# Optimization experiments

Measured on AMD Instinct MI355X. Metric: run time of the kernel, lower is better.

Reference implementation:

```python
import jax, jax.numpy as jnp
import numpy as np

N, E, B = 50000, 100000, 512   # nodes, edges, graphs
H, F_NODE, F_EDGE, T_OUT = 64, 16, 8, 1
T = 3                           # message-passing steps


def setup_inputs() -> dict:
    key = jax.random.key(0)
    ks = jax.random.split(key, 18)

    def w(k, shape, fan_in):
        return jax.random.normal(k, shape, dtype=jnp.float32) / np.sqrt(fan_in)

    return {
        "node_features": jax.random.normal(ks[0], (N, F_NODE), dtype=jnp.float32),
        "edge_features": jax.random.normal(ks[1], (E, F_EDGE), dtype=jnp.float32),
        "Esrc": jax.random.randint(ks[2], (E,), 0, N, dtype=jnp.int32),
        "Etgt": jax.random.randint(ks[3], (E,), 0, N, dtype=jnp.int32),
        "batch": jnp.sort(jax.random.randint(ks[4], (N,), 0, B, dtype=jnp.int32)),
        # input linear: node_features -> hidden
        "Win": w(ks[5], (H, F_NODE), F_NODE),
        "bin_": jnp.zeros((H,), jnp.float32),
        # edge encoder MLP: edge_features -> hidden -> hidden*hidden
        "We1": w(ks[6], (H, F_EDGE), F_EDGE),
        "be1": jnp.zeros((H,), jnp.float32),
        "We2": w(ks[7], (H * H, H), H),
        "be2": jnp.zeros((H * H,), jnp.float32),
        # GRU cell (shared across T steps)
        "Wih": w(ks[8], (3 * H, H), H),
        "bih": jnp.zeros((3 * H,), jnp.float32),
        "Whh": w(ks[9], (3 * H, H), H),
        "bhh": jnp.zeros((3 * H,), jnp.float32),
        # output linear: hidden -> target_features
        "Wout": w(ks[10], (T_OUT, H), H),
        "bout": jnp.zeros((T_OUT,), jnp.float32),
    }


def _gru(x, h, Wih, bih, Whh, bhh):
    gi = x @ Wih.T + bih            # [N, 3H]
    gh = h @ Whh.T + bhh
    i_r, i_z, i_n = jnp.split(gi, 3, axis=-1)
    h_r, h_z, h_n = jnp.split(gh, 3, axis=-1)
    r = jax.nn.sigmoid(i_r + h_r)
    z = jax.nn.sigmoid(i_z + h_z)
    n = jnp.tanh(i_n + r * h_n)
    return (1.0 - z) * n + z * h


def reference(node_features, edge_features, Esrc, Etgt, batch,
              Win, bin_, We1, be1, We2, be2,
              Wih, bih, Whh, bhh, Wout, bout):
    # Edge encoder MLP -> per-edge [H, H] message matrix (ENN style)
    eh = jax.nn.relu(edge_features @ We1.T + be1)          # [E, H]
    edge_data = (eh @ We2.T + be2).reshape(E, H, H)        # [E, H, H]

    x = node_features @ Win.T + bin_                       # [N, H]

    for _ in range(T):  # small fixed layer count
        msg = jnp.einsum('eij,ej->ei', edge_data, x[Esrc])  # per-edge matvec
        agg = jax.ops.segment_sum(msg, Etgt, num_segments=N)
        x = _gru(agg, x, Wih, bih, Whh, bhh)

    out = x @ Wout.T + bout                                # [N, 1]
    pooled = jax.ops.segment_sum(out, batch, num_segments=B)  # [B, 1]
    return pooled
```

## Files before the change

### kernel.cpp

```cpp
#include <hip/hip_runtime.h>
#include <hip/hip_fp16.h>

#define NN 50000
#define NE 100000
#define NB 512

typedef _Float16 f16x8 __attribute__((ext_vector_type(8)));
typedef _Float16 f16x4 __attribute__((ext_vector_type(4)));
typedef float f32x4  __attribute__((ext_vector_type(4)));
typedef float f32x16 __attribute__((ext_vector_type(16)));

__device__ __forceinline__ float sigm(float v) { return 1.0f / (1.0f + __expf(-v)); }
__device__ __forceinline__ float tanh_fast(float v) {
    float e = __expf(-2.0f * fabsf(v));
    float t = (1.0f - e) / (1.0f + e);
    return v < 0.f ? -t : t;
}

__global__ void fill0_kernel(float4* __restrict__ p, int n4)
{
    int i = blockIdx.x * 256 + threadIdx.x;
    const int stride = gridDim.x * 256;
    for (; i < n4; i += stride) p[i] = make_float4(0.f, 0.f, 0.f, 0.f);
}

__global__ __launch_bounds__(256) void node_in_kernel(
    const float* __restrict__ nf, const float* __restrict__ Win,
    const float* __restrict__ bin_, float* __restrict__ x, __half* __restrict__ xh)
{
    int idx = blockIdx.x * 256 + threadIdx.x;
    if (idx >= NN * 64) return;
    int n = idx >> 6, h = idx & 63;
    float acc = bin_[h];
    #pragma unroll
    for (int f = 0; f < 16; f++) acc += nf[n * 16 + f] * Win[h * 16 + f];
    x[idx] = acc;
    xh[idx] = __float2half(acc);
}

__global__ __launch_bounds__(256) void edge_l1_kernel(
    const float* __restrict__ ef, const float* __restrict__ We1,
    const float* __restrict__ be1, __half* __restrict__ ehh)
{
    int idx = blockIdx.x * 256 + threadIdx.x;
    if (idx >= NE * 64) return;
    int e = idx >> 6, k = idx & 63;
    float acc = be1[k];
    #pragma unroll
    for (int f = 0; f < 8; f++) acc += ef[e * 8 + f] * We1[k * 8 + f];
    ehh[idx] = __float2half(fmaxf(acc, 0.0f));
}

__global__ __launch_bounds__(256) void pack_b32_kernel(
    const float* __restrict__ We2, const float* __restrict__ be2,
    __half* __restrict__ Bp)
{
    int idx = blockIdx.x * 256 + threadIdx.x;
    if (idx >= 260 * 1024) return;
    int i  = idx & 7;
    int n  = (idx >> 3) & 31;
    int hi = (idx >> 8) & 1;
    int nt = (idx >> 9) & 1;
    int kt = idx >> 10;
    int p  = kt * 16 + hi * 8 + i;
    int col = nt * 32 + n;
    float v;
    if (p < 4096) {
        int j = p >> 6, k = p & 63;
        v = We2[((size_t)(col * 64 + j)) * 64 + k];
    } else {
        v = be2[col * 64 + (p - 4096)];
    }
    Bp[idx] = __float2half(v);
}

__global__ __launch_bounds__(256) void pack_gru_kernel(
    const float* __restrict__ Wih, const float* __restrict__ Whh,
    __half* __restrict__ WG)
{
    int idx = blockIdx.x * 256 + threadIdx.x;
    if (idx >= 24576) return;
    int kk = idx & 31;
    int n  = (idx >> 5) & 15;
    int nt = (idx >> 9) % 24;
    int kt = (idx >> 9) / 24;
    int k = kt * 32 + kk;
    int col192 = (nt % 12) * 16 + n;
    int gate = col192 >> 6, h = col192 & 63;
    const float* src = (nt < 12) ? Wih : Whh;
    WG[idx] = __float2half(src[((size_t)(gate * 64 + h)) * 64 + k]);
}

__global__ __launch_bounds__(256, 2) void msg_kernel(
    const __half* __restrict__ xh, const __half* __restrict__ ehh,
    const __half* __restrict__ Bp,
    const int* __restrict__ Esrc, const int* __restrict__ Etgt,
    float* __restrict__ agg)
{
    __shared__ __attribute__((aligned(16))) __half xs[256 * 72];
    __shared__ __attribute__((aligned(16))) __half bst[16 * 1024];
    __shared__ int tgt_s[256];
    const int tid = threadIdx.x;
    const int e0 = blockIdx.x * 256;
    const int w = tid >> 6, lane = tid & 63;
    const int n32 = lane & 31, hi = lane >> 5;

    {
        const int e = e0 + tid;
        const bool ok = (e < NE);
        const int src = ok ? Esrc[e] : 0;
        tgt_s[tid] = ok ? Etgt[e] : -1;
        const uint4* xsrc = (const uint4*)(xh + (size_t)src * 64);
        #pragma unroll
        for (int i = 0; i < 8; i++) {
            uint4 v = ok ? xsrc[i] : make_uint4(0, 0, 0, 0);
            *(uint4*)(&xs[tid * 72 + i * 8]) = v;
        }
    }

    __half2 ehc[2][4][4];
    #pragma unroll
    for (int mt = 0; mt < 2; mt++) {
        const int e = e0 + w * 64 + mt * 32 + n32;
        if (e < NE) {
            #pragma unroll
            for (int c4 = 0; c4 < 4; c4++) {
                union { uint4 u; __half2 h[4]; } u;
                u.u = *(const uint4*)(ehh + (size_t)e * 64 + c4 * 16 + hi * 8);
                #pragma unroll
                for (int q = 0; q < 4; q++) ehc[mt][c4][q] = u.h[q];
            }
        } else {
            __half2 z = __half2half2(__float2half(0.f));
            #pragma unroll
            for (int c4 = 0; c4 < 4; c4++)
                #pragma unroll
                for (int q = 0; q < 4; q++) ehc[mt][c4][q] = z;
        }
    }

    f32x16 acc[2][2];
    #pragma unroll
    for (int a = 0; a < 2; a++)
        #pragma unroll
        for (int b = 0; b < 2; b++)
            #pragma unroll
            for (int q = 0; q < 16; q++) acc[a][b][q] = 0.f;

    const int rowA0 = w * 64 + n32;
    const __half* blane = bst + hi * 256 + n32 * 8;

    #pragma unroll 1
    for (int c = 0; c < 17; c++) {
        const int nkt = (c < 16) ? 16 : 4;
        __syncthreads();
        {
            const __half* gsrc = Bp + (size_t)c * 16384;
            for (int i = 0; i < nkt / 2; i++)
                *(uint4*)(bst + (size_t)(i * 256 + tid) * 8) =
                    *(const uint4*)(gsrc + (size_t)(i * 256 + tid) * 8);
        }
        __syncthreads();

        if (c < 16) {
            f16x4 xr4[2];
            #pragma unroll
            for (int mt = 0; mt < 2; mt++)
                xr4[mt] = *(const f16x4*)(xs + (rowA0 + mt * 32) * 72 + c * 4);
            #pragma unroll
            for (int u = 0; u < 16; u++) {
                f16x8 b0 = *(const f16x8*)(blane + u * 1024);
                f16x8 b1 = *(const f16x8*)(blane + u * 1024 + 512);
                const int c4 = u & 3;
                const int jq = u >> 2;
                #pragma unroll
                for (int mt = 0; mt < 2; mt++) {
                    union { f16x4 v; __half h[4]; } xu; xu.v = xr4[mt];
                    __half2 xv2 = __half2half2(xu.h[jq]);
                    union { __half2 h[4]; f16x8 v; } a;
                    #pragma unroll
                    for (int q = 0; q < 4; q++) a.h[q] = __hmul2(xv2, ehc[mt][c4][q]);
                    acc[mt][0] = __builtin_amdgcn_mfma_f32_32x32x16_f16(a.v, b0, acc[mt][0], 0, 0, 0);
                    acc[mt][1] = __builtin_amdgcn_mfma_f32_32x32x16_f16(a.v, b1, acc[mt][1], 0, 0, 0);
                }
            }
        } else {
            #pragma unroll
            for (int u = 0; u < 4; u++) {
                f16x8 b0 = *(const f16x8*)(blane + u * 1024);
                f16x8 b1 = *(const f16x8*)(blane + u * 1024 + 512);
                #pragma unroll
                for (int mt = 0; mt < 2; mt++) {
                    f16x8 a = *(const f16x8*)(xs + (rowA0 + mt * 32) * 72 + u * 16 + hi * 8);
                    acc[mt][0] = __builtin_amdgcn_mfma_f32_32x32x16_f16(a, b0, acc[mt][0], 0, 0, 0);
                    acc[mt][1] = __builtin_amdgcn_mfma_f32_32x32x16_f16(a, b1, acc[mt][1], 0, 0, 0);
                }
            }
        }
    }

    #pragma unroll
    for (int mt = 0; mt < 2; mt++) {
        #pragma unroll
        for (int r = 0; r < 16; r++) {
            const int rowe = (r & 3) + 8 * (r >> 2) + 4 * hi;
            const int t = tgt_s[w * 64 + mt * 32 + rowe];
            if (t >= 0) {
                atomicAdd(agg + (size_t)t * 64 + n32, acc[mt][0][r]);
                atomicAdd(agg + (size_t)t * 64 + 32 + n32, acc[mt][1][r]);
            }
        }
    }
}

__global__ __launch_bounds__(256, 3) void gru_kernel(
    const float* __restrict__ agg, float* __restrict__ x, __half* __restrict__ xh,
    const __half* __restrict__ WG,
    const float* __restrict__ bih, const float* __restrict__ bhh)
{
    __shared__ __attribute__((aligned(16))) __half wlds[24576];
    const int tid = threadIdx.x;
    {
        const uint4* src = (const uint4*)WG;
        uint4* dst = (uint4*)wlds;
        #pragma unroll
        for (int i = 0; i < 12; i++) dst[i * 256 + tid] = src[i * 256 + tid];
    }
    __syncthreads();

    const int w = tid >> 6, lane = tid & 63, m = lane & 15, quad = lane >> 4;

    #pragma unroll 1
    for (int tile = blockIdx.x; tile < (NN + 63) / 64; tile += 512) {
        const int nbase = tile * 64 + w * 16;
        const int anode = nbase + m;
        const bool aok = (anode < NN);

        f16x8 a_agg[2], a_x[2];
        #pragma unroll
        for (int kt = 0; kt < 2; kt++) {
            const int koff = kt * 32 + quad * 8;
            if (aok) {
                const float* ap = agg + (size_t)anode * 64 + koff;
                float4 f0 = *(const float4*)ap;
                float4 f1 = *(const float4*)(ap + 4);
                union { __half2 h[4]; f16x8 v; } u;
                u.h[0] = __floats2half2_rn(f0.x, f0.y);
                u.h[1] = __floats2half2_rn(f0.z, f0.w);
                u.h[2] = __floats2half2_rn(f1.x, f1.y);
                u.h[3] = __floats2half2_rn(f1.z, f1.w);
                a_agg[kt] = u.v;
                a_x[kt] = *(const f16x8*)(xh + (size_t)anode * 64 + koff);
            } else {
                f16x8 z;
                #pragma unroll
                for (int i = 0; i < 8; i++) z[i] = (_Float16)0;
                a_agg[kt] = z; a_x[kt] = z;
            }
        }

        f32x4 acc[24];
        #pragma unroll
        for (int nt = 0; nt < 24; nt++)
            #pragma unroll
            for (int q = 0; q < 4; q++) acc[nt][q] = 0.f;

        #pragma unroll
        for (int kt = 0; kt < 2; kt++) {
            #pragma unroll
            for (int nt = 0; nt < 24; nt++) {
                f16x8 b = *(const f16x8*)(wlds + (kt * 24 + nt) * 512 + m * 32 + quad * 8);
                acc[nt] = __builtin_amdgcn_mfma_f32_16x16x32_f16(
                    (nt < 12) ? a_agg[kt] : a_x[kt], b, acc[nt], 0, 0, 0);
            }
        }

        #pragma unroll
        for (int t = 0; t < 4; t++) {
            const int h = t * 16 + m;
            const float bir = bih[h], biz = bih[64 + h], bin = bih[128 + h];
            const float bhr = bhh[h], bhz = bhh[64 + h], bhn = bhh[128 + h];
            #pragma unroll
            for (int r = 0; r < 4; r++) {
                const int nd = nbase + quad * 4 + r;
                if (nd >= NN) continue;
                float ir  = acc[t][r]      + bir;
                float iz  = acc[4 + t][r]  + biz;
                float in_ = acc[8 + t][r]  + bin;
                float hr  = acc[12 + t][r] + bhr;
                float hz  = acc[16 + t][r] + bhz;
                float hn  = acc[20 + t][r] + bhn;
                float rg = sigm(ir + hr);
                float z  = sigm(iz + hz);
                float n  = tanh_fast(in_ + rg * hn);
                float xold = x[(size_t)nd * 64 + h];
                float xn = (1.0f - z) * n + z * xold;
                x[(size_t)nd * 64 + h] = xn;
                xh[(size_t)nd * 64 + h] = __float2half(xn);
            }
        }
    }
}

__global__ __launch_bounds__(256) void pool_kernel(
    const float* __restrict__ x, const float* __restrict__ Wout,
    const float* __restrict__ bout, const int* __restrict__ batch,
    float* __restrict__ out)
{
    const int node = blockIdx.x * 256 + threadIdx.x;
    if (node >= NN) return;
    float acc = bout[0];
    const float4* xp = (const float4*)(x + (size_t)node * 64);
    #pragma unroll
    for (int i = 0; i < 16; i++) {
        float4 v = xp[i];
        acc += v.x * Wout[4*i] + v.y * Wout[4*i+1] + v.z * Wout[4*i+2] + v.w * Wout[4*i+3];
    }
    atomicAdd(out + batch[node], acc);
}

extern "C" void kernel_launch(void* const* d_in, const int* in_sizes, int n_in,
                              void* d_out, int out_size, void* d_ws, size_t ws_size,
                              hipStream_t stream)
{
    const float* nf   = (const float*)d_in[0];
    const float* ef   = (const float*)d_in[1];
    const int*   Esrc = (const int*)  d_in[2];
    const int*   Etgt = (const int*)  d_in[3];
    const int*   bat  = (const int*)  d_in[4];
    const float* Win  = (const float*)d_in[5];
    const float* bin_ = (const float*)d_in[6];
    const float* We1  = (const float*)d_in[7];
    const float* be1  = (const float*)d_in[8];
    const float* We2  = (const float*)d_in[9];
    const float* be2  = (const float*)d_in[10];
    const float* Wih  = (const float*)d_in[11];
    const float* bih  = (const float*)d_in[12];
    const float* Whh  = (const float*)d_in[13];
    const float* bhh  = (const float*)d_in[14];
    const float* Wout = (const float*)d_in[15];
    const float* bout = (const float*)d_in[16];

    char* ws = (char*)d_ws;
    float*  x   = (float*)(ws);
    float*  agg = (float*)(ws + 12800000);
    __half* xh  = (__half*)(ws + 25600000);
    __half* ehh = (__half*)(ws + 32000000);
    __half* Bp  = (__half*)(ws + 44800000);
    __half* WG  = (__half*)(ws + 45400064);

    hipMemsetAsync(d_out, 0, NB * sizeof(float), stream);

    node_in_kernel<<<(NN * 64 + 255) / 256, 256, 0, stream>>>(nf, Win, bin_, x, xh);
    edge_l1_kernel<<<(NE * 64 + 255) / 256, 256, 0, stream>>>(ef, We1, be1, ehh);
    pack_b32_kernel<<<(260 * 1024 + 255) / 256, 256, 0, stream>>>(We2, be2, Bp);
    pack_gru_kernel<<<(24576 + 255) / 256, 256, 0, stream>>>(Wih, Whh, WG);

    for (int t = 0; t < 3; t++) {
        fill0_kernel<<<1024, 256, 0, stream>>>((float4*)agg, NN * 16);
        msg_kernel<<<(NE + 255) / 256, 256, 0, stream>>>(xh, ehh, Bp, Esrc, Etgt, agg);
        gru_kernel<<<512, 256, 0, stream>>>(agg, x, xh, WG, bih, bhh);
    }

    pool_kernel<<<(NN + 255) / 256, 256, 0, stream>>>(x, Wout, bout, bat, (float*)d_out);
}
```

Before: 551.0 us.

## Shrink msg blocks to one wave and stage GRU tiles through LDS

```diff
diff --git a/kernel.cpp b/kernel.cpp
--- a/kernel.cpp
+++ b/kernel.cpp
@@ -91,37 +91,38 @@
     WG[idx] = __float2half(src[((size_t)(gate * 64 + h)) * 64 + k]);
 }
 
-__global__ __launch_bounds__(256, 2) void msg_kernel(
+__global__ __launch_bounds__(64, 1) void msg_kernel(
     const __half* __restrict__ xh, const __half* __restrict__ ehh,
     const __half* __restrict__ Bp,
     const int* __restrict__ Esrc, const int* __restrict__ Etgt,
     float* __restrict__ agg)
 {
-    __shared__ __attribute__((aligned(16))) __half xs[256 * 72];
+    __shared__ __attribute__((aligned(16))) __half xs[128 * 72];
     __shared__ __attribute__((aligned(16))) __half bst[16 * 1024];
-    __shared__ int tgt_s[256];
-    const int tid = threadIdx.x;
-    const int e0 = blockIdx.x * 256;
-    const int w = tid >> 6, lane = tid & 63;
+    __shared__ int tgt_s[128];
+    const int lane = threadIdx.x;
+    const int e0 = blockIdx.x * 128;
     const int n32 = lane & 31, hi = lane >> 5;
 
-    {
-        const int e = e0 + tid;
+    #pragma unroll
+    for (int rr = 0; rr < 2; rr++) {
+        const int row = rr * 64 + lane;
+        const int e = e0 + row;
         const bool ok = (e < NE);
         const int src = ok ? Esrc[e] : 0;
-        tgt_s[tid] = ok ? Etgt[e] : -1;
+        tgt_s[row] = ok ? Etgt[e] : -1;
         const uint4* xsrc = (const uint4*)(xh + (size_t)src * 64);
         #pragma unroll
         for (int i = 0; i < 8; i++) {
             uint4 v = ok ? xsrc[i] : make_uint4(0, 0, 0, 0);
-            *(uint4*)(&xs[tid * 72 + i * 8]) = v;
-        }
-    }
-
-    __half2 ehc[2][4][4];
-    #pragma unroll
-    for (int mt = 0; mt < 2; mt++) {
-        const int e = e0 + w * 64 + mt * 32 + n32;
+            *(uint4*)(&xs[row * 72 + i * 8]) = v;
+        }
+    }
+
+    __half2 ehc[4][4][4];
+    #pragma unroll
+    for (int mt = 0; mt < 4; mt++) {
+        const int e = e0 + mt * 32 + n32;
         if (e < NE) {
             #pragma unroll
             for (int c4 = 0; c4 < 4; c4++) {
@@ -139,34 +140,33 @@
         }
     }
 
-    f32x16 acc[2][2];
-    #pragma unroll
-    for (int a = 0; a < 2; a++)
+    f32x16 acc[4][2];
+    #pragma unroll
+    for (int a = 0; a < 4; a++)
         #pragma unroll
         for (int b = 0; b < 2; b++)
             #pragma unroll
             for (int q = 0; q < 16; q++) acc[a][b][q] = 0.f;
 
-    const int rowA0 = w * 64 + n32;
     const __half* blane = bst + hi * 256 + n32 * 8;
 
     #pragma unroll 1
     for (int c = 0; c < 17; c++) {
-        const int nkt = (c < 16) ? 16 : 4;
+        const int niter = (c < 16) ? 32 : 8;
         __syncthreads();
         {
             const __half* gsrc = Bp + (size_t)c * 16384;
-            for (int i = 0; i < nkt / 2; i++)
-                *(uint4*)(bst + (size_t)(i * 256 + tid) * 8) =
-                    *(const uint4*)(gsrc + (size_t)(i * 256 + tid) * 8);
+            for (int i = 0; i < niter; i++)
+                *(uint4*)(bst + (size_t)(i * 64 + lane) * 8) =
+                    *(const uint4*)(gsrc + (size_t)(i * 64 + lane) * 8);
         }
         __syncthreads();
 
         if (c < 16) {
-            f16x4 xr4[2];
-            #pragma unroll
-            for (int mt = 0; mt < 2; mt++)
-                xr4[mt] = *(const f16x4*)(xs + (rowA0 + mt * 32) * 72 + c * 4);
+            f16x4 xr4[4];
+            #pragma unroll
+            for (int mt = 0; mt < 4; mt++)
+                xr4[mt] = *(const f16x4*)(xs + (mt * 32 + n32) * 72 + c * 4);
             #pragma unroll
             for (int u = 0; u < 16; u++) {
                 f16x8 b0 = *(const f16x8*)(blane + u * 1024);
@@ -174,7 +174,7 @@
                 const int c4 = u & 3;
                 const int jq = u >> 2;
                 #pragma unroll
-                for (int mt = 0; mt < 2; mt++) {
+                for (int mt = 0; mt < 4; mt++) {
                     union { f16x4 v; __half h[4]; } xu; xu.v = xr4[mt];
                     __half2 xv2 = __half2half2(xu.h[jq]);
                     union { __half2 h[4]; f16x8 v; } a;
@@ -190,8 +190,8 @@
                 f16x8 b0 = *(const f16x8*)(blane + u * 1024);
                 f16x8 b1 = *(const f16x8*)(blane + u * 1024 + 512);
                 #pragma unroll
-                for (int mt = 0; mt < 2; mt++) {
-                    f16x8 a = *(const f16x8*)(xs + (rowA0 + mt * 32) * 72 + u * 16 + hi * 8);
+                for (int mt = 0; mt < 4; mt++) {
+                    f16x8 a = *(const f16x8*)(xs + (mt * 32 + n32) * 72 + u * 16 + hi * 8);
                     acc[mt][0] = __builtin_amdgcn_mfma_f32_32x32x16_f16(a, b0, acc[mt][0], 0, 0, 0);
                     acc[mt][1] = __builtin_amdgcn_mfma_f32_32x32x16_f16(a, b1, acc[mt][1], 0, 0, 0);
                 }
@@ -200,11 +200,11 @@
     }
 
     #pragma unroll
-    for (int mt = 0; mt < 2; mt++) {
+    for (int mt = 0; mt < 4; mt++) {
         #pragma unroll
         for (int r = 0; r < 16; r++) {
             const int rowe = (r & 3) + 8 * (r >> 2) + 4 * hi;
-            const int t = tgt_s[w * 64 + mt * 32 + rowe];
+            const int t = tgt_s[mt * 32 + rowe];
             if (t >= 0) {
                 atomicAdd(agg + (size_t)t * 64 + n32, acc[mt][0][r]);
                 atomicAdd(agg + (size_t)t * 64 + 32 + n32, acc[mt][1][r]);
@@ -213,91 +213,120 @@
     }
 }
 
-__global__ __launch_bounds__(256, 3) void gru_kernel(
+__global__ __launch_bounds__(256, 2) void gru_kernel(
     const float* __restrict__ agg, float* __restrict__ x, __half* __restrict__ xh,
     const __half* __restrict__ WG,
     const float* __restrict__ bih, const float* __restrict__ bhh)
 {
     __shared__ __attribute__((aligned(16))) __half wlds[24576];
+    __shared__ __attribute__((aligned(16))) __half aggh[64 * 72];
+    __shared__ __attribute__((aligned(16))) float xbuf[64 * 68];
     const int tid = threadIdx.x;
+    const int node0 = blockIdx.x * 64;
+
     {
         const uint4* src = (const uint4*)WG;
         uint4* dst = (uint4*)wlds;
         #pragma unroll
         for (int i = 0; i < 12; i++) dst[i * 256 + tid] = src[i * 256 + tid];
     }
+    #pragma unroll
+    for (int i = 0; i < 4; i++) {
+        int idx4 = i * 256 + tid;
+        int nl = idx4 >> 4, c4 = idx4 & 15;
+        int node = node0 + nl;
+        float4 a = make_float4(0.f, 0.f, 0.f, 0.f);
+        float4 xv = make_float4(0.f, 0.f, 0.f, 0.f);
+        if (node < NN) {
+            a  = *(const float4*)(agg + (size_t)node * 64 + c4 * 4);
+            xv = *(const float4*)(x   + (size_t)node * 64 + c4 * 4);
+        }
+        __half2* ah = (__half2*)(aggh + nl * 72 + c4 * 4);
+        ah[0] = __floats2half2_rn(a.x, a.y);
+        ah[1] = __floats2half2_rn(a.z, a.w);
+        *(float4*)(xbuf + nl * 68 + c4 * 4) = xv;
+    }
     __syncthreads();
 
     const int w = tid >> 6, lane = tid & 63, m = lane & 15, quad = lane >> 4;
-
-    #pragma unroll 1
-    for (int tile = blockIdx.x; tile < (NN + 63) / 64; tile += 512) {
-        const int nbase = tile * 64 + w * 16;
-        const int anode = nbase + m;
-        const bool aok = (anode < NN);
-
-        f16x8 a_agg[2], a_x[2];
-        #pragma unroll
-        for (int kt = 0; kt < 2; kt++) {
-            const int koff = kt * 32 + quad * 8;
-            if (aok) {
-                const float* ap = agg + (size_t)anode * 64 + koff;
-                float4 f0 = *(const float4*)ap;
-                float4 f1 = *(const float4*)(ap + 4);
-                union { __half2 h[4]; f16x8 v; } u;
-                u.h[0] = __floats2half2_rn(f0.x, f0.y);
-                u.h[1] = __floats2half2_rn(f0.z, f0.w);
-                u.h[2] = __floats2half2_rn(f1.x, f1.y);
-                u.h[3] = __floats2half2_rn(f1.z, f1.w);
-                a_agg[kt] = u.v;
-                a_x[kt] = *(const f16x8*)(xh + (size_t)anode * 64 + koff);
-            } else {
-                f16x8 z;
-                #pragma unroll
-                for (int i = 0; i < 8; i++) z[i] = (_Float16)0;
-                a_agg[kt] = z; a_x[kt] = z;
-            }
-        }
-
-        f32x4 acc[24];
-        #pragma unroll
-        for (int nt = 0; nt < 24; nt++)
-            #pragma unroll
-            for (int q = 0; q < 4; q++) acc[nt][q] = 0.f;
-
-        #pragma unroll
-        for (int kt = 0; kt < 2; kt++) {
-            #pragma unroll
-            for (int nt = 0; nt < 24; nt++) {
-                f16x8 b = *(const f16x8*)(wlds + (kt * 24 + nt) * 512 + m * 32 + quad * 8);
-                acc[nt] = __builtin_amdgcn_mfma_f32_16x16x32_f16(
-                    (nt < 12) ? a_agg[kt] : a_x[kt], b, acc[nt], 0, 0, 0);
-            }
-        }
-
-        #pragma unroll
-        for (int t = 0; t < 4; t++) {
-            const int h = t * 16 + m;
-            const float bir = bih[h], biz = bih[64 + h], bin = bih[128 + h];
-            const float bhr = bhh[h], bhz = bhh[64 + h], bhn = bhh[128 + h];
-            #pragma unroll
-            for (int r = 0; r < 4; r++) {
-                const int nd = nbase + quad * 4 + r;
-                if (nd >= NN) continue;
-                float ir  = acc[t][r]      + bir;
-                float iz  = acc[4 + t][r]  + biz;
-                float in_ = acc[8 + t][r]  + bin;
-                float hr  = acc[12 + t][r] + bhr;
-                float hz  = acc[16 + t][r] + bhz;
-                float hn  = acc[20 + t][r] + bhn;
-                float rg = sigm(ir + hr);
-                float z  = sigm(iz + hz);
-                float n  = tanh_fast(in_ + rg * hn);
-                float xold = x[(size_t)nd * 64 + h];
-                float xn = (1.0f - z) * n + z * xold;
-                x[(size_t)nd * 64 + h] = xn;
-                xh[(size_t)nd * 64 + h] = __float2half(xn);
-            }
+    const int nl_a = w * 16 + m;
+
+    f16x8 a_agg[2], a_x[2];
+    #pragma unroll
+    for (int kt = 0; kt < 2; kt++) {
+        const int koff = kt * 32 + quad * 8;
+        a_agg[kt] = *(const f16x8*)(aggh + nl_a * 72 + koff);
+        const float* xp = xbuf + nl_a * 68 + koff;
+        union { __half2 h[4]; f16x8 v; } u;
+        u.h[0] = __floats2half2_rn(xp[0], xp[1]);
+        u.h[1] = __floats2half2_rn(xp[2], xp[3]);
+        u.h[2] = __floats2half2_rn(xp[4], xp[5]);
+        u.h[3] = __floats2half2_rn(xp[6], xp[7]);
+        a_x[kt] = u.v;
+    }
+
+    f32x4 acc[24];
+    #pragma unroll
+    for (int nt = 0; nt < 24; nt++)
+        #pragma unroll
+        for (int q = 0; q < 4; q++) acc[nt][q] = 0.f;
+
+    #pragma unroll
+    for (int kt = 0; kt < 2; kt++) {
+        #pragma unroll
+        for (int nt = 0; nt < 24; nt++) {
+            f16x8 b = *(const f16x8*)(wlds + (kt * 24 + nt) * 512 + m * 32 + quad * 8);
+            acc[nt] = __builtin_amdgcn_mfma_f32_16x16x32_f16(
+                (nt < 12) ? a_agg[kt] : a_x[kt], b, acc[nt], 0, 0, 0);
+        }
+    }
+
+    #pragma unroll
+    for (int t = 0; t < 4; t++) {
+        const int h = t * 16 + m;
+        const float bir = bih[h], biz = bih[64 + h], bin = bih[128 + h];
+        const float bhr = bhh[h], bhz = bhh[64 + h], bhn = bhh[128 + h];
+        #pragma unroll
+        for (int r = 0; r < 4; r++) {
+            const int nl = w * 16 + quad * 4 + r;
+            float ir  = acc[t][r]      + bir;
+            float iz  = acc[4 + t][r]  + biz;
+            float in_ = acc[8 + t][r]  + bin;
+            float hr  = acc[12 + t][r] + bhr;
+            float hz  = acc[16 + t][r] + bhz;
+            float hn  = acc[20 + t][r] + bhn;
+            float rg = sigm(ir + hr);
+            float z  = sigm(iz + hz);
+            float n  = tanh_fast(in_ + rg * hn);
+            float xold = xbuf[nl * 68 + h];
+            xbuf[nl * 68 + h] = (1.0f - z) * n + z * xold;
+        }
+    }
+    __syncthreads();
+
+    #pragma unroll
+    for (int i = 0; i < 4; i++) {
+        int idx4 = i * 256 + tid;
+        int nl = idx4 >> 4, c4 = idx4 & 15;
+        int node = node0 + nl;
+        if (node < NN) {
+            float4 v = *(const float4*)(xbuf + nl * 68 + c4 * 4);
+            *(float4*)(x + (size_t)node * 64 + c4 * 4) = v;
+        }
+    }
+    #pragma unroll
+    for (int i = 0; i < 2; i++) {
+        int idx8 = i * 256 + tid;
+        int nl = idx8 >> 3, c8 = idx8 & 7;
+        int node = node0 + nl;
+        if (node < NN) {
+            const float* xp = xbuf + nl * 68 + c8 * 8;
+            union { __half2 h[4]; uint4 u; } u;
+            u.h[0] = __floats2half2_rn(xp[0], xp[1]);
+            u.h[1] = __floats2half2_rn(xp[2], xp[3]);
+            u.h[2] = __floats2half2_rn(xp[4], xp[5]);
+            u.h[3] = __floats2half2_rn(xp[6], xp[7]);
+            *(uint4*)(xh + (size_t)node * 64 + c8 * 8) = u.u;
         }
     }
 }
@@ -358,8 +387,8 @@
 
     for (int t = 0; t < 3; t++) {
         fill0_kernel<<<1024, 256, 0, stream>>>((float4*)agg, NN * 16);
-        msg_kernel<<<(NE + 255) / 256, 256, 0, stream>>>(xh, ehh, Bp, Esrc, Etgt, agg);
-        gru_kernel<<<512, 256, 0, stream>>>(agg, x, xh, WG, bih, bhh);
+        msg_kernel<<<(NE + 127) / 128, 64, 0, stream>>>(xh, ehh, Bp, Esrc, Etgt, agg);
+        gru_kernel<<<(NN + 63) / 64, 256, 0, stream>>>(agg, x, xh, WG, bih, bhh);
     }
 
     pool_kernel<<<(NN + 255) / 256, 256, 0, stream>>>(x, Wout, bout, bat, (float*)d_out);
```

New measurement: 699.4 us. +26.9%, slower.
